# Kernel optimization log

Hardware: AMD Instinct MI355X
Metric: run time of the kernel (lower is better)

The kernel has to match this reference:

```python
import jax, jax.numpy as jnp
import numpy as np
from jax import lax

NPG = 61      # nodes (electrodes) per graph, hard-coded by 61*hidden reshape
B = 128       # graphs per batch
L = 160       # raw signal length -> final conv length 1
NF = 64       # num_features
HC = 128      # hidden_channels
NCLS = 4


def setup_inputs() -> dict:
    key = jax.random.key(0)
    ks = jax.random.split(key, 16)
    N = B * NPG
    # fully-connected (no self-loops) edges within each graph -> 3660 edges/graph
    a = np.repeat(np.arange(NPG), NPG)
    b = np.tile(np.arange(NPG), NPG)
    m = a != b
    sl, dl = a[m], b[m]
    off = (np.arange(B) * NPG)[:, None]
    edge_index = np.stack([(sl[None] + off).ravel(), (dl[None] + off).ravel()]).astype(np.int64)
    batch = np.repeat(np.arange(B), NPG).astype(np.int64)

    def rn(k, shape, fan_in):
        return jax.random.normal(k, shape, jnp.float32) / np.sqrt(fan_in).astype(np.float32)

    return dict(
        x=jax.random.normal(ks[0], (N, L), jnp.float32),
        edge_index=jnp.asarray(edge_index),
        batch=jnp.asarray(batch),
        edge_features=jax.random.normal(ks[1], (edge_index.shape[1], 3), jnp.float32),
        conv_w0=rn(ks[2], (NF, 1, 7), 7.0), conv_b0=jnp.zeros((NF,), jnp.float32),
        conv_w1=rn(ks[3], (NF, NF, 5), NF * 5.0), conv_b1=jnp.zeros((NF,), jnp.float32),
        conv_w2=rn(ks[4], (NF, NF, 3), NF * 3.0), conv_b2=jnp.zeros((NF,), jnp.float32),
        bn1_g=jnp.ones((NF,), jnp.float32), bn1_b=jnp.zeros((NF,), jnp.float32),
        g_w0=rn(ks[5], (NF, HC), float(NF)), g_b0=jnp.zeros((HC,), jnp.float32),
        g_w1=rn(ks[6], (HC, HC), float(HC)), g_b1=jnp.zeros((HC,), jnp.float32),
        g_w2=rn(ks[7], (HC, HC), float(HC)), g_b2=jnp.zeros((HC,), jnp.float32),
        bn2_g=jnp.ones((HC,), jnp.float32), bn2_b=jnp.zeros((HC,), jnp.float32),
        lin_w0=rn(ks[8], (NPG * HC, HC), float(NPG * HC)), lin_b0=jnp.zeros((HC,), jnp.float32),
        lin_w1=rn(ks[9], (HC, HC), float(HC)), lin_b1=jnp.zeros((HC,), jnp.float32),
        lin_w2=rn(ks[10], (HC, NCLS), float(HC)), lin_b2=jnp.zeros((NCLS,), jnp.float32),
        edge_w=rn(ks[11], (3, 1), 3.0), edge_b=jnp.zeros((1,), jnp.float32),
    )


def _conv1d(x, w, b, pad):
    # x: [N, Cin, L], w: [Cout, Cin, K]
    y = lax.conv_general_dilated(x, w, (1,), [(pad, pad)], dimension_numbers=('NCH', 'OIH', 'NCH'))
    return y + b[None, :, None]


def _maxpool7(x):
    n = x.shape[-1] // 7
    return x[..., : n * 7].reshape(x.shape[0], x.shape[1], n, 7).max(-1)


def _bn(x, g, b):
    # BatchNorm1d in training mode: biased batch statistics
    m = x.mean(0)
    v = x.var(0)
    return (x - m) * lax.rsqrt(v + 1e-5) * g + b


def _forward(x, edge_features, conv_w0, conv_b0, conv_w1, conv_b1, conv_w2, conv_b2,
             bn1_g, bn1_b, g_w0, g_b0, g_w1, g_b1, g_w2, g_b2, bn2_g, bn2_b,
             lin_w0, lin_b0, lin_w1, lin_b1, lin_w2, lin_b2, edge_w, edge_b,
             edge_index, batch):
    N = x.shape[0]
    nb = N // NPG  # == batch.max()+1 for contiguous graph layout
    # tanh-gated edge weights
    ew = jnp.tanh(edge_features @ edge_w + edge_b)            # [E, 1]
    # Conv1d feature extractor: [N,1,160] -> [N,NF,1]
    h = x[:, None, :]
    h = _maxpool7(jax.nn.relu(_conv1d(h, conv_w0, conv_b0, 0)))   # [N,NF,22]
    h = jax.nn.relu(_conv1d(h, conv_w1, conv_b1, 2))               # [N,NF,22]
    h = _maxpool7(h)                                               # [N,NF,3]
    h = _conv1d(h, conv_w2, conv_b2, 0)[:, :, 0]                   # [N,NF]
    h = _bn(h, bn1_g, bn1_b)
    # Edge-weighted GCN hops (MyzConv): lin -> gather src -> scale -> scatter-add dst
    src, dst = edge_index[0], edge_index[1]
    for w, bs, act in ((g_w0, g_b0, True), (g_w1, g_b1, True), (g_w2, g_b2, False)):
        hw = h @ w + bs                                            # [N,HC]
        msg = ew * hw[src]                                         # [E,HC]
        h = jax.ops.segment_sum(msg, dst, num_segments=N)
        if act:
            h = jax.nn.relu(h)
    h = _bn(h, bn2_g, bn2_b)
    # MLP classifier over concatenated node features per graph
    h = h.reshape(nb, NPG * HC)
    h = jax.nn.relu(h @ lin_w0 + lin_b0)
    h = jax.nn.relu(h @ lin_w1 + lin_b1)
    h = h @ lin_w2 + lin_b2
    return jax.nn.log_softmax(h, -1), ew.reshape(nb, -1).T


def reference(x, edge_index, batch, edge_features, conv_w0, conv_b0, conv_w1, conv_b1,
              conv_w2, conv_b2, bn1_g, bn1_b, g_w0, g_b0, g_w1, g_b1, g_w2, g_b2,
              bn2_g, bn2_b, lin_w0, lin_b0, lin_w1, lin_b1, lin_w2, lin_b2, edge_w, edge_b):
    return _forward(x, edge_features, conv_w0, conv_b0, conv_w1, conv_b1, conv_w2, conv_b2,
                    bn1_g, bn1_b, g_w0, g_b0, g_w1, g_b1, g_w2, g_b2, bn2_g, bn2_b,
                    lin_w0, lin_b0, lin_w1, lin_b1, lin_w2, lin_b2, edge_w, edge_b,
                    edge_index, batch)
```

## Files before the change

### kernel.cpp

```cpp
#include <hip/hip_runtime.h>
#include <math.h>

#define NPGN 61
#define NGRAPH 128
#define NNODES (NPGN*NGRAPH)
#define EPG 3660

typedef float float4v __attribute__((ext_vector_type(4)));
typedef short bf16x8 __attribute__((ext_vector_type(8)));
typedef unsigned short u16;

__device__ __forceinline__ u16 f2bf(float v){
  union { float f; unsigned u; } x; x.f = v;
  unsigned r = (x.u + 0x7FFFu + ((x.u >> 16) & 1u)) >> 16;
  return (u16)r;
}
__device__ __forceinline__ float bf2f(unsigned u){
  union { unsigned u; float f; } x; x.u = u << 16;
  return x.f;
}

__global__ __launch_bounds__(256) void k_prep(const float* __restrict__ w0,
    const float* __restrict__ w1, const float* __restrict__ w2,
    const float* __restrict__ gw0, const float* __restrict__ gw1, const float* __restrict__ gw2,
    const float* __restrict__ lw0,
    float* __restrict__ w0t, u16* __restrict__ w1b, u16* __restrict__ w2b,
    u16* __restrict__ gwt0, u16* __restrict__ gwt1, u16* __restrict__ gwt2,
    u16* __restrict__ lw0t){
  __shared__ __align__(16) u16 tile[32*132];
  int b = blockIdx.x, tid = threadIdx.x;
  if (b < 290){
    int idx = b*256 + tid;
    if (idx < 20480){
      int f = idx / 320, r = idx - f*320;
      int kk = r >> 6, c = r & 63;
      w1b[idx] = f2bf(w1[f*320 + c*5 + kk]);
    } else if (idx < 32768){
      int j = idx - 20480; w2b[j] = f2bf(w2[j]);
    } else if (idx < 40960){
      int j = idx - 32768; int jj = j >> 6, k = j & 63; gwt0[j] = f2bf(gw0[k*128 + jj]);
    } else if (idx < 57344){
      int j = idx - 40960; int jj = j >> 7, k = j & 127; gwt1[j] = f2bf(gw1[k*128 + jj]);
    } else if (idx < 73728){
      int j = idx - 57344; int jj = j >> 7, k = j & 127; gwt2[j] = f2bf(gw2[k*128 + jj]);
    } else if (idx < 74176){
      int j = idx - 73728; int k = j >> 6, f = j & 63; w0t[j] = w0[f*7 + k];
    }
  } else {
    int bb = b - 290;
    int i = bb >> 2, oq = bb & 3;
    for (int idx = tid; idx < 4096; idx += 256){
      int k = idx >> 5, ol = idx & 31;
      tile[ol*132 + k] = f2bf(lw0[((size_t)i*128 + k)*128 + oq*32 + ol]);
    }
    __syncthreads();
    unsigned* dst = (unsigned*)lw0t;
    for (int idx = tid; idx < 2048; idx += 256){
      int ol = idx >> 6, kw = idx & 63;
      unsigned v = (unsigned)tile[ol*132 + 2*kw] | ((unsigned)tile[ol*132 + 2*kw + 1] << 16);
      dst[((size_t)i*128 + oq*32 + ol)*64 + kw] = v;
    }
  }
}

#define A0T_STR 72
#define C1_STR 24
#define NB 4
__global__ __launch_bounds__(256) void k_conv(const float* __restrict__ x,
    const float* __restrict__ w0t, const float* __restrict__ b0,
    const u16* __restrict__ w1b, const float* __restrict__ b1,
    const u16* __restrict__ w2b, const float* __restrict__ b2,
    float* __restrict__ h0, float* __restrict__ stat1p){
  int w = threadIdx.x >> 6, lane = threadIdx.x & 63;
  int tid = threadIdx.x;
  int q = lane >> 4, r16 = lane & 15;
  __shared__ __align__(16) float xs[NB][160];
  __shared__ __align__(16) u16 a0t[NB][36*A0T_STR];
  __shared__ __align__(16) u16 c1s[NB][64*C1_STR];
  __shared__ __align__(16) u16 a1k[NB][208];

  {
    const float* xb = x + (size_t)blockIdx.x*NB*160;
    float* xsf = &xs[0][0];
    #pragma unroll
    for (int idx = tid; idx < NB*160; idx += 256) xsf[idx] = xb[idx];
  }

  bf16x8 wf1[10], wf2[6];
  #pragma unroll
  for (int ks = 0; ks < 10; ks++)
    wf1[ks] = *(const bf16x8*)(w1b + (16*w + r16)*320 + ks*32 + q*8);
  #pragma unroll
  for (int ks = 0; ks < 6; ks++)
    wf2[ks] = *(const bf16x8*)(w2b + (16*w + r16)*192 + ks*32 + q*8);
  float4 b1v = *(const float4*)(b1 + 16*w + 4*q);
  float4 b2v = *(const float4*)(b2 + 16*w + 4*q);

  float w0r[7];
  #pragma unroll
  for (int k = 0; k < 7; k++) w0r[k] = w0t[k*64 + lane];
  float b0f = b0[lane];

  #pragma unroll
  for (int i2 = 0; i2 < 6; i2++){
    int rp = (i2 < 2) ? i2 : 22 + i2;
    a0t[w][rp*A0T_STR + lane] = 0;
  }
  __syncthreads();

  for (int j = w; j < 44; j += 4){
    int n = j / 11, qp = j - n*11;
    const float* xsp = &xs[n][0];
    float win[20];
// ... 20 lines not shown
  __syncthreads();

  #pragma unroll 1
  for (int n = 0; n < NB; n++){
    float4v acc0 = {0.f,0.f,0.f,0.f}, acc1 = {0.f,0.f,0.f,0.f};
    #pragma unroll
    for (int ks = 0; ks < 10; ks++){
      int kk = ks >> 1;
      int cbase = (ks & 1)*32 + q*8;
      bf16x8 bv0 = *(const bf16x8*)(&a0t[n][(r16 + kk)*A0T_STR + cbase]);
      bf16x8 bv1 = *(const bf16x8*)(&a0t[n][(r16 + 16 + kk)*A0T_STR + cbase]);
      acc0 = __builtin_amdgcn_mfma_f32_16x16x32_bf16(wf1[ks], bv0, acc0, 0, 0, 0);
      acc1 = __builtin_amdgcn_mfma_f32_16x16x32_bf16(wf1[ks], bv1, acc1, 0, 0, 0);
    }
    #pragma unroll
    for (int reg = 0; reg < 4; reg++){
      int m = 16*w + q*4 + reg;
      float bv_ = ((const float*)&b1v)[reg];
      c1s[n][m*C1_STR + r16] = f2bf(fmaxf(acc0[reg] + bv_, 0.f));
      if (r16 <= 4)
        c1s[n][m*C1_STR + 16 + r16] = f2bf(fmaxf(acc1[reg] + bv_, 0.f));
    }
  }
  __syncthreads();

  {
    const u16* c1 = &c1s[w][0];
    bf16x8 f0 = *(const bf16x8*)(c1 + lane*C1_STR);
    bf16x8 f1 = *(const bf16x8*)(c1 + lane*C1_STR + 8);
    bf16x8 f2 = *(const bf16x8*)(c1 + lane*C1_STR + 16);
    float v[24];
    #pragma unroll
    for (int j = 0; j < 8; j++){
      v[j]    = bf2f((u16)f0[j]);
      v[8+j]  = bf2f((u16)f1[j]);
      v[16+j] = bf2f((u16)f2[j]);
    }
    #pragma unroll
    for (int t = 0; t < 3; t++){
      float m = v[t*7];
      #pragma unroll
      for (int r = 1; r < 7; r++) m = fmaxf(m, v[t*7+r]);
      a1k[w][lane*3 + t] = f2bf(m);
    }
  }
  __syncthreads();

  float4v sacc = {0.f,0.f,0.f,0.f}, qacc = {0.f,0.f,0.f,0.f};
  #pragma unroll 1
  for (int n = 0; n < NB; n++){
    float4v acc2 = {0.f,0.f,0.f,0.f};
    #pragma unroll
    for (int ks = 0; ks < 6; ks++){
      bf16x8 bs = *(const bf16x8*)(&a1k[n][ks*32 + q*8]);
      acc2 = __builtin_amdgcn_mfma_f32_16x16x32_bf16(wf2[ks], bs, acc2, 0, 0, 0);
    }
    if (r16 == 0){
      int nn = blockIdx.x*NB + n;
      #pragma unroll
      for (int reg = 0; reg < 4; reg++){
        int f = 16*w + 4*q + reg;
        float v = acc2[reg] + ((const float*)&b2v)[reg];
        h0[(size_t)nn*64 + f] = v;
        sacc[reg] += v;
        qacc[reg] += v*v;
      }
    }
  }

  if (r16 == 0){
    int bkt = blockIdx.x & 31;
    #pragma unroll
    for (int reg = 0; reg < 4; reg++){
      int f = 16*w + 4*q + reg;
      atomicAdd(&stat1p[bkt*128 + f], sacc[reg]);
      atomicAdd(&stat1p[bkt*128 + 64 + f], qacc[reg]);
    }
  }
}

#define EW_STR 72
#define HS_STR 136
#define HWT_STR 72
__global__ __launch_bounds__(512) void k_gnn(const float* __restrict__ h0,
    const float* __restrict__ stat1p,
    const float* __restrict__ bn1g, const float* __restrict__ bn1b,
    const u16* __restrict__ gwt0, const float* __restrict__ gb0,
    const u16* __restrict__ gwt1, const float* __restrict__ gb1,
    const u16* __restrict__ gwt2, const float* __restrict__ gb2,
    const float* __restrict__ ef, const float* __restrict__ eww,
    const float* __restrict__ ewb, float* __restrict__ out2,
    u16* __restrict__ hB, float* __restrict__ stat2p){
  int g = blockIdx.x, tid = threadIdx.x;
  int w = tid >> 6, lane = tid & 63, q = lane >> 4, r16 = lane & 15;
  int dt = w & 3, jh = w >> 2;
  __shared__ u16 hs[64*HS_STR];
  __shared__ u16 hwT[128*HWT_STR];
  __shared__ u16 ewl[64*EW_STR];
  __shared__ float bsc[64], bsh[64];
  __shared__ float st2[256];

  bf16x8 af0[2], af1[4], af2[4];
  #pragma unroll
  for (int ks = 0; ks < 2; ks++)
    af0[ks] = *(const bf16x8*)(gwt0 + (16*w + r16)*64 + ks*32 + q*8);
  #pragma unroll
  for (int ks = 0; ks < 4; ks++)
    af1[ks] = *(const bf16x8*)(gwt1 + (16*w + r16)*128 + ks*32 + q*8);
  #pragma unroll
  for (int ks = 0; ks < 4; ks++)
    af2[ks] = *(const bf16x8*)(gwt2 + (16*w + r16)*128 + ks*32 + q*8);
  float4 b40 = *(const float4*)(gb0 + 16*w + 4*q);
  float4 b41 = *(const float4*)(gb1 + 16*w + 4*q);
  float4 b42 = *(const float4*)(gb2 + 16*w + 4*q);

  if (tid < 64){
    float s = 0.f, s2 = 0.f;
    #pragma unroll
    for (int r = 0; r < 32; r++){
      s  += stat1p[r*128 + tid];
      s2 += stat1p[r*128 + 64 + tid];
    }
    float m = s*(1.f/NNODES), v = s2*(1.f/NNODES) - m*m;
    float sc = rsqrtf(v + 1e-5f)*bn1g[tid];
    bsc[tid] = sc; bsh[tid] = bn1b[tid] - m*sc;
  }
  if (tid < 256) st2[tid] = 0.f;
  {
    unsigned* td = (unsigned*)ewl;
    for (int idx = tid; idx < 64*EW_STR/2; idx += 512) td[idx] = 0;
  }
  {
    unsigned* hsd = (unsigned*)hs;
    for (int idx = tid; idx < 3*(HS_STR/2); idx += 512){
      int rr = 61 + idx/(HS_STR/2), cc = idx%(HS_STR/2);
      hsd[rr*(HS_STR/2) + cc] = 0;
    }
  }
  __syncthreads();

  {
    float v0 = eww[0], v1 = eww[1], v2 = eww[2], bb = ewb[0];
    const float* efg = ef + (size_t)g*EPG*3;
    for (int idx = tid; idx < EPG; idx += 512){
      const float* p = efg + idx*3;
      float v = tanhf(p[0]*v0 + p[1]*v1 + p[2]*v2 + bb);
      int s = idx/60, r = idx - s*60;
      int d = r + (r >= s ? 1 : 0);
      ewl[d*EW_STR + s] = f2bf(v);
      out2[(size_t)idx*128 + g] = v;
    }
  }
  {
    unsigned* hsd = (unsigned*)hs;
    for (int idx = tid; idx < 61*32; idx += 512){
      int i = idx >> 5, kw = idx & 31;
      float2 hv = *(const float2*)(h0 + ((size_t)g*61 + i)*64 + kw*2);
      int k0 = kw*2;
      float a = hv.x*bsc[k0] + bsh[k0];
      float b = hv.y*bsc[k0+1] + bsh[k0+1];
      hsd[i*(HS_STR/2) + kw] = (unsigned)f2bf(a) | ((unsigned)f2bf(b) << 16);
    }
  }
  __syncthreads();
  bf16x8 ewf[2];
  #pragma unroll
  for (int ks = 0; ks < 2; ks++)
    ewf[ks] = *(const bf16x8*)(ewl + (16*dt + r16)*EW_STR + ks*32 + q*8);

  #pragma unroll
  for (int nt = 0; nt < 4; nt++){
    float4v acc = {b40.x, b40.y, b40.z, b40.w};
    #pragma unroll
    for (int ks = 0; ks < 2; ks++){
      bf16x8 bv = *(const bf16x8*)(hs + (nt*16 + r16)*HS_STR + ks*32 + q*8);
      acc = __builtin_amdgcn_mfma_f32_16x16x32_bf16(af0[ks], bv, acc, 0, 0, 0);
    }
    #pragma unroll
    for (int r = 0; r < 4; r++)
      hwT[(16*w + 4*q + r)*HWT_STR + nt*16 + r16] = f2bf(acc[r]);
  }
  __syncthreads();
  #pragma unroll
  for (int nt = 0; nt < 4; nt++){
    int j = (jh*4 + nt)*16;
    float4v acc = {0.f,0.f,0.f,0.f};
    #pragma unroll
    for (int ks = 0; ks < 2; ks++){
      bf16x8 bv = *(const bf16x8*)(hwT + (j + r16)*HWT_STR + ks*32 + q*8);
      acc = __builtin_amdgcn_mfma_f32_16x16x32_bf16(ewf[ks], bv, acc, 0, 0, 0);
    }
    #pragma unroll
    for (int r = 0; r < 4; r++){
      int d = 16*dt + 4*q + r;
      hs[d*HS_STR + j + r16] = f2bf(fmaxf(acc[r], 0.f));
    }
  }
  __syncthreads();

  #pragma unroll
  for (int nt = 0; nt < 4; nt++){
    float4v acc = {b41.x, b41.y, b41.z, b41.w};
    #pragma unroll
    for (int ks = 0; ks < 4; ks++){
      bf16x8 bv = *(const bf16x8*)(hs + (nt*16 + r16)*HS_STR + ks*32 + q*8);
      acc = __builtin_amdgcn_mfma_f32_16x16x32_bf16(af1[ks], bv, acc, 0, 0, 0);
    }
    #pragma unroll
    for (int r = 0; r < 4; r++)
      hwT[(16*w + 4*q + r)*HWT_STR + nt*16 + r16] = f2bf(acc[r]);
  }
  __syncthreads();
  #pragma unroll
  for (int nt = 0; nt < 4; nt++){
    int j = (jh*4 + nt)*16;
    float4v acc = {0.f,0.f,0.f,0.f};
    #pragma unroll
    for (int ks = 0; ks < 2; ks++){
      bf16x8 bv = *(const bf16x8*)(hwT + (j + r16)*HWT_STR + ks*32 + q*8);
      acc = __builtin_amdgcn_mfma_f32_16x16x32_bf16(ewf[ks], bv, acc, 0, 0, 0);
    }
    #pragma unroll
    for (int r = 0; r < 4; r++){
      int d = 16*dt + 4*q + r;
      hs[d*HS_STR + j + r16] = f2bf(fmaxf(acc[r], 0.f));
    }
  }
  __syncthreads();

  #pragma unroll
  for (int nt = 0; nt < 4; nt++){
    float4v acc = {b42.x, b42.y, b42.z, b42.w};
    #pragma unroll
    for (int ks = 0; ks < 4; ks++){
      bf16x8 bv = *(const bf16x8*)(hs + (nt*16 + r16)*HS_STR + ks*32 + q*8);
      acc = __builtin_amdgcn_mfma_f32_16x16x32_bf16(af2[ks], bv, acc, 0, 0, 0);
    }
    #pragma unroll
    for (int r = 0; r < 4; r++)
      hwT[(16*w + 4*q + r)*HWT_STR + nt*16 + r16] = f2bf(acc[r]);
  }
  __syncthreads();
  #pragma unroll
  for (int nt = 0; nt < 4; nt++){
    int j = (jh*4 + nt)*16;
    float4v acc = {0.f,0.f,0.f,0.f};
    #pragma unroll
    for (int ks = 0; ks < 2; ks++){
      bf16x8 bv = *(const bf16x8*)(hwT + (j + r16)*HWT_STR + ks*32 + q*8);
      acc = __builtin_amdgcn_mfma_f32_16x16x32_bf16(ewf[ks], bv, acc, 0, 0, 0);
    }
    float cs = 0.f, cq = 0.f;
    #pragma unroll
    for (int r = 0; r < 4; r++){
      int d = 16*dt + 4*q + r;
      if (d < 61){
        float v = acc[r];
        hB[((size_t)g*61 + d)*128 + j + r16] = f2bf(v);
        cs += v; cq += v*v;
      }
    }
    int col = j + r16;
    atomicAdd(&st2[col], cs);
    atomicAdd(&st2[128 + col], cq);
  }
  __syncthreads();
  if (tid < 256) stat2p[(size_t)tid*128 + g] = st2[tid];
}

#define AS_STR 136
__global__ __launch_bounds__(256) void k_mlp0(const u16* __restrict__ hB,
    const float* __restrict__ stat2p,
    const float* __restrict__ bn2g, const float* __restrict__ bn2b,
    const u16* __restrict__ lw0t, float* __restrict__ y0pre){
  int bi = blockIdx.x; int i = bi >> 2, sub = bi & 3;
  int oh = sub & 1, gh = sub >> 1;
  int tid = threadIdx.x, w = tid >> 6, lane = tid & 63, q = lane >> 4, r16 = lane & 15;
  __shared__ u16 As[64*AS_STR];
  __shared__ float sc2[128], sh2[128];
  if (tid < 128){
    float4v sa = {0,0,0,0}, sb = {0,0,0,0};
    #pragma unroll
    for (int r = 0; r < 32; r++){
      sa += *(const float4v*)(stat2p + (size_t)tid*128 + r*4);
      sb += *(const float4v*)(stat2p + (size_t)(128 + tid)*128 + r*4);
    }
    float s = sa[0]+sa[1]+sa[2]+sa[3], s2 = sb[0]+sb[1]+sb[2]+sb[3];
    float m = s*(1.f/NNODES), v = s2*(1.f/NNODES) - m*m;
    float sc = rsqrtf(v + 1e-5f)*bn2g[tid];
    sc2[tid] = sc; sh2[tid] = bn2b[tid] - m*sc;
  }
  __syncthreads();
  {
    const unsigned* hbd = (const unsigned*)hB;
    unsigned* asd = (unsigned*)As;
    for (int idx = tid; idx < 4096; idx += 256){
      int gg = gh*64 + (idx >> 6), kw = idx & 63;
      unsigned pv = hbd[((size_t)gg*61 + i)*64 + kw];
      int k0 = kw*2;
      float a = bf2f(pv & 0xffffu)*sc2[k0] + sh2[k0];
      float b = bf2f(pv >> 16)*sc2[k0+1] + sh2[k0+1];
      asd[(idx >> 6)*(AS_STR/2) + kw] = (unsigned)f2bf(a) | ((unsigned)f2bf(b) << 16);
    }
  }
  __syncthreads();
  const u16* wbase = lw0t + ((size_t)i*128 + oh*64)*128;
  bf16x8 af[4];
  #pragma unroll
  for (int ks = 0; ks < 4; ks++)
    af[ks] = *(const bf16x8*)(As + (16*w + r16)*AS_STR + ks*32 + q*8);
  #pragma unroll
  for (int nt = 0; nt < 4; nt++){
    float4v acc = {0.f,0.f,0.f,0.f};
    #pragma unroll
    for (int ks = 0; ks < 4; ks++){
      bf16x8 bv = *(const bf16x8*)(wbase + (size_t)(nt*16 + r16)*128 + ks*32 + q*8);
      acc = __builtin_amdgcn_mfma_f32_16x16x32_bf16(af[ks], bv, acc, 0, 0, 0);
    }
    #pragma unroll
    for (int r = 0; r < 4; r++){
      int g = gh*64 + 16*w + 4*q + r;
      atomicAdd(&y0pre[(size_t)g*128 + oh*64 + nt*16 + r16], acc[r]);
    }
  }
}

__global__ __launch_bounds__(128) void k_mlp1(const float* __restrict__ y0pre,
    const float* __restrict__ lb0, const float* __restrict__ W1,
    const float* __restrict__ lb1, const float* __restrict__ W2,
    const float* __restrict__ lb2, float* __restrict__ out){
  int g = blockIdx.x, o = threadIdx.x;
  __shared__ float y0[128], y1[128], red[128];
  y0[o] = fmaxf(y0pre[(size_t)g*128 + o] + lb0[o], 0.f);
  __syncthreads();
  float a = lb1[o];
  #pragma unroll 8
  for (int k = 0; k < 128; k++) a += y0[k]*W1[k*128 + o];
  y1[o] = fmaxf(a, 0.f);
  __syncthreads();
  int c = o & 3, kb = o >> 2;
  float a2 = 0.f;
  #pragma unroll
  for (int j = 0; j < 4; j++){
    int k = kb + 32*j;
    a2 += y1[k]*W2[k*4 + c];
  }
  red[o] = a2;
  __syncthreads();
  #pragma unroll
  for (int off = 64; off >= 4; off >>= 1){
    if (o < off) red[o] += red[o + off];
    __syncthreads();
  }
  if (o == 0){
    float v0 = red[0]+lb2[0], v1 = red[1]+lb2[1], v2 = red[2]+lb2[2], v3 = red[3]+lb2[3];
    float m = fmaxf(fmaxf(v0,v1), fmaxf(v2,v3));
    float lse = m + logf(expf(v0-m)+expf(v1-m)+expf(v2-m)+expf(v3-m));
    out[g*4+0]=v0-lse; out[g*4+1]=v1-lse; out[g*4+2]=v2-lse; out[g*4+3]=v3-lse;
  }
}

extern "C" void kernel_launch(void* const* d_in, const int* in_sizes, int n_in,
                              void* d_out, int out_size, void* d_ws, size_t ws_size,
                              hipStream_t stream){
  const float* x    = (const float*)d_in[0];
  const float* ef   = (const float*)d_in[3];
  const float* cw0  = (const float*)d_in[4];
  const float* cb0  = (const float*)d_in[5];
  const float* cw1  = (const float*)d_in[6];
  const float* cb1  = (const float*)d_in[7];
  const float* cw2  = (const float*)d_in[8];
  const float* cb2  = (const float*)d_in[9];
  const float* bn1g = (const float*)d_in[10];
  const float* bn1b = (const float*)d_in[11];
  const float* gw0  = (const float*)d_in[12];
  const float* gb0  = (const float*)d_in[13];
  const float* gw1  = (const float*)d_in[14];
  const float* gb1  = (const float*)d_in[15];
  const float* gw2  = (const float*)d_in[16];
  const float* gb2  = (const float*)d_in[17];
  const float* bn2g = (const float*)d_in[18];
  const float* bn2b = (const float*)d_in[19];
  const float* lw0  = (const float*)d_in[20];
  const float* lb0  = (const float*)d_in[21];
  const float* lw1  = (const float*)d_in[22];
  const float* lb1  = (const float*)d_in[23];
  const float* lw2  = (const float*)d_in[24];
  const float* lb2  = (const float*)d_in[25];
  const float* eww  = (const float*)d_in[26];
  const float* ewb  = (const float*)d_in[27];
  float* out = (float*)d_out;

  float* ws   = (float*)d_ws;
  float* w1s  = ws;
  float* w2s  = w1s + 10240;
  float* w0t  = w2s + 6144;
  float* gws0 = w0t + 448;
  float* gws1 = gws0 + 4096;
  float* gws2 = gws1 + 8192;
  float* h0   = gws2 + 8192;
  float* hBs  = h0 + 499712;
  float* lw0s = hBs + 499712;
  float* accs = lw0s + 499712;

  u16* w1b    = (u16*)w1s;
  u16* w2b    = (u16*)w2s;
  u16* gwt0   = (u16*)gws0;
  u16* gwt1   = (u16*)gws1;
  u16* gwt2   = (u16*)gws2;
  u16* hB     = (u16*)hBs;
  u16* lw0t   = (u16*)lw0s;
  float* stat1p = accs;
  float* y0pre  = accs + 4096;
  float* stat2p = accs + 20480;

  hipMemsetAsync(accs, 0, 20480*sizeof(float), stream);
  k_prep <<<534, 256, 0, stream>>>(cw0, cw1, cw2, gw0, gw1, gw2, lw0,
                                   w0t, w1b, w2b, gwt0, gwt1, gwt2, lw0t);
  k_conv <<<NNODES/NB, 256, 0, stream>>>(x, w0t, cb0, w1b, cb1, w2b, cb2, h0, stat1p);
  k_gnn  <<<NGRAPH, 512, 0, stream>>>(h0, stat1p, bn1g, bn1b,
                                      gwt0, gb0, gwt1, gb1, gwt2, gb2,
                                      ef, eww, ewb, out + 512, hB, stat2p);
  k_mlp0 <<<NPGN*4, 256, 0, stream>>>(hB, stat2p, bn2g, bn2b, lw0t, y0pre);
  k_mlp1 <<<NGRAPH, 128, 0, stream>>>(y0pre, lb0, lw1, lb1, lw2, lb2, out);
}
```

Measured before the change: 199.1 us.

## Fuse GNN and MLP stages into one cooperative kernel with grid syncs

The separate GNN, first-MLP and second-MLP kernels are merged into a single cooperative kernel with 244 blocks, separated by grid-wide barriers. The accumulator memset moves into extra blocks of the prep kernel. The aim is to remove launch gaps and the memset launch. The costs are grid-sync latency, idle blocks during the GNN and final phases, and larger shared-memory use per block from the union of all stages, which may limit co-residency.

```diff
diff --git a/kernel.cpp b/kernel.cpp
--- a/kernel.cpp
+++ b/kernel.cpp
@@ -1,5 +1,8 @@
 #include <hip/hip_runtime.h>
+#include <hip/hip_cooperative_groups.h>
 #include <math.h>
+
+namespace cg = cooperative_groups;
 
 #define NPGN 61
 #define NGRAPH 128
@@ -26,9 +29,14 @@
     const float* __restrict__ lw0,
     float* __restrict__ w0t, u16* __restrict__ w1b, u16* __restrict__ w2b,
     u16* __restrict__ gwt0, u16* __restrict__ gwt1, u16* __restrict__ gwt2,
-    u16* __restrict__ lw0t){
+    u16* __restrict__ lw0t, float* __restrict__ accs){
   __shared__ __align__(16) u16 tile[32*132];
   int b = blockIdx.x, tid = threadIdx.x;
+  if (b >= 534){
+    int idx = (b - 534)*256 + tid;
+    if (idx < 20480) accs[idx] = 0.f;
+    return;
+  }
   if (b < 290){
     int idx = b*256 + tid;
     if (idx < 20480){
@@ -215,281 +223,295 @@
 #define EW_STR 72
 #define HS_STR 136
 #define HWT_STR 72
-__global__ __launch_bounds__(512) void k_gnn(const float* __restrict__ h0,
+#define AS_STR 136
+__global__ __launch_bounds__(512) void k_tail(const float* __restrict__ h0,
     const float* __restrict__ stat1p,
     const float* __restrict__ bn1g, const float* __restrict__ bn1b,
     const u16* __restrict__ gwt0, const float* __restrict__ gb0,
     const u16* __restrict__ gwt1, const float* __restrict__ gb1,
     const u16* __restrict__ gwt2, const float* __restrict__ gb2,
     const float* __restrict__ ef, const float* __restrict__ eww,
-    const float* __restrict__ ewb, float* __restrict__ out2,
-    u16* __restrict__ hB, float* __restrict__ stat2p){
-  int g = blockIdx.x, tid = threadIdx.x;
+    const float* __restrict__ ewb, u16* __restrict__ hB,
+    float* __restrict__ stat2p,
+    const float* __restrict__ bn2g, const float* __restrict__ bn2b,
+    const u16* __restrict__ lw0t, float* __restrict__ y0pre,
+    const float* __restrict__ lb0, const float* __restrict__ W1,
+    const float* __restrict__ lb1, const float* __restrict__ W2,
+    const float* __restrict__ lb2, float* __restrict__ out){
+  int tid = threadIdx.x;
   int w = tid >> 6, lane = tid & 63, q = lane >> 4, r16 = lane & 15;
-  int dt = w & 3, jh = w >> 2;
   __shared__ u16 hs[64*HS_STR];
   __shared__ u16 hwT[128*HWT_STR];
   __shared__ u16 ewl[64*EW_STR];
   __shared__ float bsc[64], bsh[64];
   __shared__ float st2[256];
-
-  bf16x8 af0[2], af1[4], af2[4];
-  #pragma unroll
-  for (int ks = 0; ks < 2; ks++)
-    af0[ks] = *(const bf16x8*)(gwt0 + (16*w + r16)*64 + ks*32 + q*8);
-  #pragma unroll
-  for (int ks = 0; ks < 4; ks++)
-    af1[ks] = *(const bf16x8*)(gwt1 + (16*w + r16)*128 + ks*32 + q*8);
-  #pragma unroll
-  for (int ks = 0; ks < 4; ks++)
-    af2[ks] = *(const bf16x8*)(gwt2 + (16*w + r16)*128 + ks*32 + q*8);
-  float4 b40 = *(const float4*)(gb0 + 16*w + 4*q);
-  float4 b41 = *(const float4*)(gb1 + 16*w + 4*q);
-  float4 b42 = *(const float4*)(gb2 + 16*w + 4*q);
-
-  if (tid < 64){
-    float s = 0.f, s2 = 0.f;
-    #pragma unroll
-    for (int r = 0; r < 32; r++){
-      s  += stat1p[r*128 + tid];
-      s2 += stat1p[r*128 + 64 + tid];
-    }
-    float m = s*(1.f/NNODES), v = s2*(1.f/NNODES) - m*m;
-    float sc = rsqrtf(v + 1e-5f)*bn1g[tid];
-    bsc[tid] = sc; bsh[tid] = bn1b[tid] - m*sc;
-  }
-  if (tid < 256) st2[tid] = 0.f;
-  {
-    unsigned* td = (unsigned*)ewl;
-    for (int idx = tid; idx < 64*EW_STR/2; idx += 512) td[idx] = 0;
-  }
-  {
-    unsigned* hsd = (unsigned*)hs;
-    for (int idx = tid; idx < 3*(HS_STR/2); idx += 512){
-      int rr = 61 + idx/(HS_STR/2), cc = idx%(HS_STR/2);
-      hsd[rr*(HS_STR/2) + cc] = 0;
-    }
-  }
-  __syncthreads();
-
-  {
-    float v0 = eww[0], v1 = eww[1], v2 = eww[2], bb = ewb[0];
-    const float* efg = ef + (size_t)g*EPG*3;
-    for (int idx = tid; idx < EPG; idx += 512){
-      const float* p = efg + idx*3;
-      float v = tanhf(p[0]*v0 + p[1]*v1 + p[2]*v2 + bb);
-      int s = idx/60, r = idx - s*60;
-      int d = r + (r >= s ? 1 : 0);
-      ewl[d*EW_STR + s] = f2bf(v);
-      out2[(size_t)idx*128 + g] = v;
-    }
-  }
-  {
-    unsigned* hsd = (unsigned*)hs;
-    for (int idx = tid; idx < 61*32; idx += 512){
-      int i = idx >> 5, kw = idx & 31;
-      float2 hv = *(const float2*)(h0 + ((size_t)g*61 + i)*64 + kw*2);
-      int k0 = kw*2;
-      float a = hv.x*bsc[k0] + bsh[k0];
-      float b = hv.y*bsc[k0+1] + bsh[k0+1];
-      hsd[i*(HS_STR/2) + kw] = (unsigned)f2bf(a) | ((unsigned)f2bf(b) << 16);
-    }
-  }
-  __syncthreads();
-  bf16x8 ewf[2];
-  #pragma unroll
-  for (int ks = 0; ks < 2; ks++)
-    ewf[ks] = *(const bf16x8*)(ewl + (16*dt + r16)*EW_STR + ks*32 + q*8);
-
-  #pragma unroll
-  for (int nt = 0; nt < 4; nt++){
-    float4v acc = {b40.x, b40.y, b40.z, b40.w};
-    #pragma unroll
-    for (int ks = 0; ks < 2; ks++){
-      bf16x8 bv = *(const bf16x8*)(hs + (nt*16 + r16)*HS_STR + ks*32 + q*8);
-      acc = __builtin_amdgcn_mfma_f32_16x16x32_bf16(af0[ks], bv, acc, 0, 0, 0);
-    }
-    #pragma unroll
-    for (int r = 0; r < 4; r++)
-      hwT[(16*w + 4*q + r)*HWT_STR + nt*16 + r16] = f2bf(acc[r]);
-  }
-  __syncthreads();
-  #pragma unroll
-  for (int nt = 0; nt < 4; nt++){
-    int j = (jh*4 + nt)*16;
-    float4v acc = {0.f,0.f,0.f,0.f};
-    #pragma unroll
-    for (int ks = 0; ks < 2; ks++){
-      bf16x8 bv = *(const bf16x8*)(hwT + (j + r16)*HWT_STR + ks*32 + q*8);
-      acc = __builtin_amdgcn_mfma_f32_16x16x32_bf16(ewf[ks], bv, acc, 0, 0, 0);
-    }
-    #pragma unroll
-    for (int r = 0; r < 4; r++){
-      int d = 16*dt + 4*q + r;
-      hs[d*HS_STR + j + r16] = f2bf(fmaxf(acc[r], 0.f));
-    }
-  }
-  __syncthreads();
-
-  #pragma unroll
-  for (int nt = 0; nt < 4; nt++){
-    float4v acc = {b41.x, b41.y, b41.z, b41.w};
-    #pragma unroll
-    for (int ks = 0; ks < 4; ks++){
-      bf16x8 bv = *(const bf16x8*)(hs + (nt*16 + r16)*HS_STR + ks*32 + q*8);
-      acc = __builtin_amdgcn_mfma_f32_16x16x32_bf16(af1[ks], bv, acc, 0, 0, 0);
-    }
-    #pragma unroll
-    for (int r = 0; r < 4; r++)
-      hwT[(16*w + 4*q + r)*HWT_STR + nt*16 + r16] = f2bf(acc[r]);
-  }
-  __syncthreads();
-  #pragma unroll
-  for (int nt = 0; nt < 4; nt++){
-    int j = (jh*4 + nt)*16;
-    float4v acc = {0.f,0.f,0.f,0.f};
-    #pragma unroll
-    for (int ks = 0; ks < 2; ks++){
-      bf16x8 bv = *(const bf16x8*)(hwT + (j + r16)*HWT_STR + ks*32 + q*8);
-      acc = __builtin_amdgcn_mfma_f32_16x16x32_bf16(ewf[ks], bv, acc, 0, 0, 0);
-    }
-    #pragma unroll
-    for (int r = 0; r < 4; r++){
-      int d = 16*dt + 4*q + r;
-      hs[d*HS_STR + j + r16] = f2bf(fmaxf(acc[r], 0.f));
-    }
-  }
-  __syncthreads();
-
-  #pragma unroll
-  for (int nt = 0; nt < 4; nt++){
-    float4v acc = {b42.x, b42.y, b42.z, b42.w};
-    #pragma unroll
-    for (int ks = 0; ks < 4; ks++){
-      bf16x8 bv = *(const bf16x8*)(hs + (nt*16 + r16)*HS_STR + ks*32 + q*8);
-      acc = __builtin_amdgcn_mfma_f32_16x16x32_bf16(af2[ks], bv, acc, 0, 0, 0);
-    }
-    #pragma unroll
-    for (int r = 0; r < 4; r++)
-      hwT[(16*w + 4*q + r)*HWT_STR + nt*16 + r16] = f2bf(acc[r]);
-  }
-  __syncthreads();
-  #pragma unroll
-  for (int nt = 0; nt < 4; nt++){
-    int j = (jh*4 + nt)*16;
-    float4v acc = {0.f,0.f,0.f,0.f};
-    #pragma unroll
-    for (int ks = 0; ks < 2; ks++){
-      bf16x8 bv = *(const bf16x8*)(hwT + (j + r16)*HWT_STR + ks*32 + q*8);
-      acc = __builtin_amdgcn_mfma_f32_16x16x32_bf16(ewf[ks], bv, acc, 0, 0, 0);
-    }
-    float cs = 0.f, cq = 0.f;
-    #pragma unroll
-    for (int r = 0; r < 4; r++){
-      int d = 16*dt + 4*q + r;
-      if (d < 61){
-        float v = acc[r];
-        hB[((size_t)g*61 + d)*128 + j + r16] = f2bf(v);
-        cs += v; cq += v*v;
-      }
-    }
-    int col = j + r16;
-    atomicAdd(&st2[col], cs);
-    atomicAdd(&st2[128 + col], cq);
-  }
-  __syncthreads();
-  if (tid < 256) stat2p[(size_t)tid*128 + g] = st2[tid];
-}
-
-#define AS_STR 136
-__global__ __launch_bounds__(256) void k_mlp0(const u16* __restrict__ hB,
-    const float* __restrict__ stat2p,
-    const float* __restrict__ bn2g, const float* __restrict__ bn2b,
-    const u16* __restrict__ lw0t, float* __restrict__ y0pre){
-  int bi = blockIdx.x; int i = bi >> 2, sub = bi & 3;
-  int oh = sub & 1, gh = sub >> 1;
-  int tid = threadIdx.x, w = tid >> 6, lane = tid & 63, q = lane >> 4, r16 = lane & 15;
   __shared__ u16 As[64*AS_STR];
   __shared__ float sc2[128], sh2[128];
-  if (tid < 128){
-    float4v sa = {0,0,0,0}, sb = {0,0,0,0};
-    #pragma unroll
-    for (int r = 0; r < 32; r++){
-      sa += *(const float4v*)(stat2p + (size_t)tid*128 + r*4);
-      sb += *(const float4v*)(stat2p + (size_t)(128 + tid)*128 + r*4);
-    }
-    float s = sa[0]+sa[1]+sa[2]+sa[3], s2 = sb[0]+sb[1]+sb[2]+sb[3];
-    float m = s*(1.f/NNODES), v = s2*(1.f/NNODES) - m*m;
-    float sc = rsqrtf(v + 1e-5f)*bn2g[tid];
-    sc2[tid] = sc; sh2[tid] = bn2b[tid] - m*sc;
-  }
-  __syncthreads();
+  __shared__ float y0[128], y1[128], red[128];
+  float* out2 = out + 512;
+
+  if (blockIdx.x < NGRAPH){
+    int g = blockIdx.x;
+    int dt = w & 3, jh = w >> 2;
+
+    bf16x8 af0[2], af1[4], af2[4];
+    #pragma unroll
+    for (int ks = 0; ks < 2; ks++)
+      af0[ks] = *(const bf16x8*)(gwt0 + (16*w + r16)*64 + ks*32 + q*8);
+    #pragma unroll
+    for (int ks = 0; ks < 4; ks++)
+      af1[ks] = *(const bf16x8*)(gwt1 + (16*w + r16)*128 + ks*32 + q*8);
+    #pragma unroll
+    for (int ks = 0; ks < 4; ks++)
+      af2[ks] = *(const bf16x8*)(gwt2 + (16*w + r16)*128 + ks*32 + q*8);
+    float4 b40 = *(const float4*)(gb0 + 16*w + 4*q);
+    float4 b41 = *(const float4*)(gb1 + 16*w + 4*q);
+    float4 b42 = *(const float4*)(gb2 + 16*w + 4*q);
+
+    if (tid < 64){
+      float s = 0.f, s2 = 0.f;
+      #pragma unroll
+      for (int r = 0; r < 32; r++){
+        s  += stat1p[r*128 + tid];
+        s2 += stat1p[r*128 + 64 + tid];
+      }
+      float m = s*(1.f/NNODES), v = s2*(1.f/NNODES) - m*m;
+      float sc = rsqrtf(v + 1e-5f)*bn1g[tid];
+      bsc[tid] = sc; bsh[tid] = bn1b[tid] - m*sc;
+    }
+    if (tid < 256) st2[tid] = 0.f;
+    {
+      unsigned* td = (unsigned*)ewl;
+      for (int idx = tid; idx < 64*EW_STR/2; idx += 512) td[idx] = 0;
+    }
+    {
+      unsigned* hsd = (unsigned*)hs;
+      for (int idx = tid; idx < 3*(HS_STR/2); idx += 512){
+        int rr = 61 + idx/(HS_STR/2), cc = idx%(HS_STR/2);
+        hsd[rr*(HS_STR/2) + cc] = 0;
+      }
+    }
+    __syncthreads();
+
+    {
+      float v0 = eww[0], v1 = eww[1], v2 = eww[2], bb = ewb[0];
+      const float* efg = ef + (size_t)g*EPG*3;
+      for (int idx = tid; idx < EPG; idx += 512){
+        const float* p = efg + idx*3;
+        float v = tanhf(p[0]*v0 + p[1]*v1 + p[2]*v2 + bb);
+        int s = idx/60, r = idx - s*60;
+        int d = r + (r >= s ? 1 : 0);
+        ewl[d*EW_STR + s] = f2bf(v);
+        out2[(size_t)idx*128 + g] = v;
+      }
+    }
+    {
+      unsigned* hsd = (unsigned*)hs;
+      for (int idx = tid; idx < 61*32; idx += 512){
+        int i = idx >> 5, kw = idx & 31;
+        float2 hv = *(const float2*)(h0 + ((size_t)g*61 + i)*64 + kw*2);
+        int k0 = kw*2;
+        float a = hv.x*bsc[k0] + bsh[k0];
+        float b = hv.y*bsc[k0+1] + bsh[k0+1];
+        hsd[i*(HS_STR/2) + kw] = (unsigned)f2bf(a) | ((unsigned)f2bf(b) << 16);
+      }
+    }
+    __syncthreads();
+    bf16x8 ewf[2];
+    #pragma unroll
+    for (int ks = 0; ks < 2; ks++)
+      ewf[ks] = *(const bf16x8*)(ewl + (16*dt + r16)*EW_STR + ks*32 + q*8);
+
+    #pragma unroll
+    for (int nt = 0; nt < 4; nt++){
+      float4v acc = {b40.x, b40.y, b40.z, b40.w};
+      #pragma unroll
+      for (int ks = 0; ks < 2; ks++){
+        bf16x8 bv = *(const bf16x8*)(hs + (nt*16 + r16)*HS_STR + ks*32 + q*8);
+        acc = __builtin_amdgcn_mfma_f32_16x16x32_bf16(af0[ks], bv, acc, 0, 0, 0);
+      }
+      #pragma unroll
+      for (int r = 0; r < 4; r++)
+        hwT[(16*w + 4*q + r)*HWT_STR + nt*16 + r16] = f2bf(acc[r]);
+    }
+    __syncthreads();
+    #pragma unroll
+    for (int nt = 0; nt < 4; nt++){
+      int j = (jh*4 + nt)*16;
+      float4v acc = {0.f,0.f,0.f,0.f};
+      #pragma unroll
+      for (int ks = 0; ks < 2; ks++){
+        bf16x8 bv = *(const bf16x8*)(hwT + (j + r16)*HWT_STR + ks*32 + q*8);
+        acc = __builtin_amdgcn_mfma_f32_16x16x32_bf16(ewf[ks], bv, acc, 0, 0, 0);
+      }
+      #pragma unroll
+      for (int r = 0; r < 4; r++){
+        int d = 16*dt + 4*q + r;
+        hs[d*HS_STR + j + r16] = f2bf(fmaxf(acc[r], 0.f));
+      }
+    }
+    __syncthreads();
+
+    #pragma unroll
+    for (int nt = 0; nt < 4; nt++){
+      float4v acc = {b41.x, b41.y, b41.z, b41.w};
+      #pragma unroll
+      for (int ks = 0; ks < 4; ks++){
+        bf16x8 bv = *(const bf16x8*)(hs + (nt*16 + r16)*HS_STR + ks*32 + q*8);
+        acc = __builtin_amdgcn_mfma_f32_16x16x32_bf16(af1[ks], bv, acc, 0, 0, 0);
+      }
+      #pragma unroll
+      for (int r = 0; r < 4; r++)
+        hwT[(16*w + 4*q + r)*HWT_STR + nt*16 + r16] = f2bf(acc[r]);
+    }
+    __syncthreads();
+    #pragma unroll
+    for (int nt = 0; nt < 4; nt++){
+      int j = (jh*4 + nt)*16;
+      float4v acc = {0.f,0.f,0.f,0.f};
+      #pragma unroll
+      for (int ks = 0; ks < 2; ks++){
+        bf16x8 bv = *(const bf16x8*)(hwT + (j + r16)*HWT_STR + ks*32 + q*8);
+        acc = __builtin_amdgcn_mfma_f32_16x16x32_bf16(ewf[ks], bv, acc, 0, 0, 0);
+      }
+      #pragma unroll
+      for (int r = 0; r < 4; r++){
+        int d = 16*dt + 4*q + r;
+        hs[d*HS_STR + j + r16] = f2bf(fmaxf(acc[r], 0.f));
+      }
+    }
+    __syncthreads();
+
+    #pragma unroll
+    for (int nt = 0; nt < 4; nt++){
+      float4v acc = {b42.x, b42.y, b42.z, b42.w};
+      #pragma unroll
+      for (int ks = 0; ks < 4; ks++){
+        bf16x8 bv = *(const bf16x8*)(hs + (nt*16 + r16)*HS_STR + ks*32 + q*8);
+        acc = __builtin_amdgcn_mfma_f32_16x16x32_bf16(af2[ks], bv, acc, 0, 0, 0);
+      }
+      #pragma unroll
+      for (int r = 0; r < 4; r++)
+        hwT[(16*w + 4*q + r)*HWT_STR + nt*16 + r16] = f2bf(acc[r]);
+    }
+    __syncthreads();
+    #pragma unroll
+    for (int nt = 0; nt < 4; nt++){
+      int j = (jh*4 + nt)*16;
+      float4v acc = {0.f,0.f,0.f,0.f};
+      #pragma unroll
+      for (int ks = 0; ks < 2; ks++){
+        bf16x8 bv = *(const bf16x8*)(hwT + (j + r16)*HWT_STR + ks*32 + q*8);
+        acc = __builtin_amdgcn_mfma_f32_16x16x32_bf16(ewf[ks], bv, acc, 0, 0, 0);
+      }
+      float cs = 0.f, cq = 0.f;
+      #pragma unroll
+      for (int r = 0; r < 4; r++){
+        int d = 16*dt + 4*q + r;
+        if (d < 61){
+          float v = acc[r];
+          hB[((size_t)g*61 + d)*128 + j + r16] = f2bf(v);
+          cs += v; cq += v*v;
+        }
+      }
+      int col = j + r16;
+      atomicAdd(&st2[col], cs);
+      atomicAdd(&st2[128 + col], cq);
+    }
+    __syncthreads();
+    if (tid < 256) stat2p[(size_t)tid*128 + g] = st2[tid];
+  }
+
+  cg::this_grid().sync();
+
   {
-    const unsigned* hbd = (const unsigned*)hB;
-    unsigned* asd = (unsigned*)As;
-    for (int idx = tid; idx < 4096; idx += 256){
-      int gg = gh*64 + (idx >> 6), kw = idx & 63;
-      unsigned pv = hbd[((size_t)gg*61 + i)*64 + kw];
-      int k0 = kw*2;
-      float a = bf2f(pv & 0xffffu)*sc2[k0] + sh2[k0];
-      float b = bf2f(pv >> 16)*sc2[k0+1] + sh2[k0+1];
-      asd[(idx >> 6)*(AS_STR/2) + kw] = (unsigned)f2bf(a) | ((unsigned)f2bf(b) << 16);
-    }
-  }
-  __syncthreads();
-  const u16* wbase = lw0t + ((size_t)i*128 + oh*64)*128;
-  bf16x8 af[4];
-  #pragma unroll
-  for (int ks = 0; ks < 4; ks++)
-    af[ks] = *(const bf16x8*)(As + (16*w + r16)*AS_STR + ks*32 + q*8);
-  #pragma unroll
-  for (int nt = 0; nt < 4; nt++){
-    float4v acc = {0.f,0.f,0.f,0.f};
-    #pragma unroll
-    for (int ks = 0; ks < 4; ks++){
-      bf16x8 bv = *(const bf16x8*)(wbase + (size_t)(nt*16 + r16)*128 + ks*32 + q*8);
-      acc = __builtin_amdgcn_mfma_f32_16x16x32_bf16(af[ks], bv, acc, 0, 0, 0);
-    }
-    #pragma unroll
-    for (int r = 0; r < 4; r++){
-      int g = gh*64 + 16*w + 4*q + r;
-      atomicAdd(&y0pre[(size_t)g*128 + oh*64 + nt*16 + r16], acc[r]);
-    }
-  }
-}
-
-__global__ __launch_bounds__(128) void k_mlp1(const float* __restrict__ y0pre,
-    const float* __restrict__ lb0, const float* __restrict__ W1,
-    const float* __restrict__ lb1, const float* __restrict__ W2,
-    const float* __restrict__ lb2, float* __restrict__ out){
-  int g = blockIdx.x, o = threadIdx.x;
-  __shared__ float y0[128], y1[128], red[128];
-  y0[o] = fmaxf(y0pre[(size_t)g*128 + o] + lb0[o], 0.f);
-  __syncthreads();
-  float a = lb1[o];
-  #pragma unroll 8
-  for (int k = 0; k < 128; k++) a += y0[k]*W1[k*128 + o];
-  y1[o] = fmaxf(a, 0.f);
-  __syncthreads();
-  int c = o & 3, kb = o >> 2;
-  float a2 = 0.f;
-  #pragma unroll
-  for (int j = 0; j < 4; j++){
-    int k = kb + 32*j;
-    a2 += y1[k]*W2[k*4 + c];
-  }
-  red[o] = a2;
-  __syncthreads();
-  #pragma unroll
-  for (int off = 64; off >= 4; off >>= 1){
-    if (o < off) red[o] += red[o + off];
-    __syncthreads();
-  }
-  if (o == 0){
-    float v0 = red[0]+lb2[0], v1 = red[1]+lb2[1], v2 = red[2]+lb2[2], v3 = red[3]+lb2[3];
-    float m = fmaxf(fmaxf(v0,v1), fmaxf(v2,v3));
-    float lse = m + logf(expf(v0-m)+expf(v1-m)+expf(v2-m)+expf(v3-m));
-    out[g*4+0]=v0-lse; out[g*4+1]=v1-lse; out[g*4+2]=v2-lse; out[g*4+3]=v3-lse;
+    int nh = w >> 2, w4 = w & 3;
+    if (tid < 128){
+      float4v sa = {0,0,0,0}, sb = {0,0,0,0};
+      #pragma unroll
+      for (int r = 0; r < 32; r++){
+        sa += *(const float4v*)(stat2p + (size_t)tid*128 + r*4);
+        sb += *(const float4v*)(stat2p + (size_t)(128 + tid)*128 + r*4);
+      }
+      float s = sa[0]+sa[1]+sa[2]+sa[3], s2 = sb[0]+sb[1]+sb[2]+sb[3];
+      float m = s*(1.f/NNODES), v = s2*(1.f/NNODES) - m*m;
+      float sc = rsqrtf(v + 1e-5f)*bn2g[tid];
+      sc2[tid] = sc; sh2[tid] = bn2b[tid] - m*sc;
+    }
+    int vb = blockIdx.x;
+    int i = vb >> 2, sub = vb & 3;
+    int oh = sub & 1, gh = sub >> 1;
+    __syncthreads();
+    {
+      const unsigned* hbd = (const unsigned*)hB;
+      unsigned* asd = (unsigned*)As;
+      for (int idx = tid; idx < 4096; idx += 512){
+        int gg = gh*64 + (idx >> 6), kw = idx & 63;
+        unsigned pv = hbd[((size_t)gg*61 + i)*64 + kw];
+        int k0 = kw*2;
+        float a = bf2f(pv & 0xffffu)*sc2[k0] + sh2[k0];
+        float b = bf2f(pv >> 16)*sc2[k0+1] + sh2[k0+1];
+        asd[(idx >> 6)*(AS_STR/2) + kw] = (unsigned)f2bf(a) | ((unsigned)f2bf(b) << 16);
+      }
+    }
+    __syncthreads();
+    const u16* wbase = lw0t + ((size_t)i*128 + oh*64)*128;
+    bf16x8 af[4];
+    #pragma unroll
+    for (int ks = 0; ks < 4; ks++)
+      af[ks] = *(const bf16x8*)(As + (16*w4 + r16)*AS_STR + ks*32 + q*8);
+    #pragma unroll
+    for (int t = 0; t < 2; t++){
+      int nt = nh*2 + t;
+      float4v acc = {0.f,0.f,0.f,0.f};
+      #pragma unroll
+      for (int ks = 0; ks < 4; ks++){
+        bf16x8 bv = *(const bf16x8*)(wbase + (size_t)(nt*16 + r16)*128 + ks*32 + q*8);
+        acc = __builtin_amdgcn_mfma_f32_16x16x32_bf16(af[ks], bv, acc, 0, 0, 0);
+      }
+      #pragma unroll
+      for (int r = 0; r < 4; r++){
+        int g = gh*64 + 16*w4 + 4*q + r;
+        atomicAdd(&y0pre[(size_t)g*128 + oh*64 + nt*16 + r16], acc[r]);
+      }
+    }
+  }
+
+  cg::this_grid().sync();
+
+  if (blockIdx.x < NGRAPH){
+    int g = blockIdx.x, o = tid;
+    if (o < 128) y0[o] = fmaxf(y0pre[(size_t)g*128 + o] + lb0[o], 0.f);
+    __syncthreads();
+    if (o < 128){
+      float a = lb1[o];
+      #pragma unroll 8
+      for (int k = 0; k < 128; k++) a += y0[k]*W1[k*128 + o];
+      y1[o] = fmaxf(a, 0.f);
+    }
+    __syncthreads();
+    if (o < 128){
+      int c = o & 3, kb = o >> 2;
+      float a2 = 0.f;
+      #pragma unroll
+      for (int j = 0; j < 4; j++){
+        int k = kb + 32*j;
+        a2 += y1[k]*W2[k*4 + c];
+      }
+      red[o] = a2;
+    }
+    __syncthreads();
+    #pragma unroll
+    for (int off = 64; off >= 4; off >>= 1){
+      if (o < off) red[o] += red[o + off];
+      __syncthreads();
+    }
+    if (o == 0){
+      float v0 = red[0]+lb2[0], v1 = red[1]+lb2[1], v2 = red[2]+lb2[2], v3 = red[3]+lb2[3];
+      float m = fmaxf(fmaxf(v0,v1), fmaxf(v2,v3));
+      float lse = m + logf(expf(v0-m)+expf(v1-m)+expf(v2-m)+expf(v3-m));
+      out[g*4+0]=v0-lse; out[g*4+1]=v1-lse; out[g*4+2]=v2-lse; out[g*4+3]=v3-lse;
+    }
   }
 }
 
@@ -547,13 +569,18 @@
   float* y0pre  = accs + 4096;
   float* stat2p = accs + 20480;
 
-  hipMemsetAsync(accs, 0, 20480*sizeof(float), stream);
-  k_prep <<<534, 256, 0, stream>>>(cw0, cw1, cw2, gw0, gw1, gw2, lw0,
-                                   w0t, w1b, w2b, gwt0, gwt1, gwt2, lw0t);
+  k_prep <<<614, 256, 0, stream>>>(cw0, cw1, cw2, gw0, gw1, gw2, lw0,
+                                   w0t, w1b, w2b, gwt0, gwt1, gwt2, lw0t, accs);
   k_conv <<<NNODES/NB, 256, 0, stream>>>(x, w0t, cb0, w1b, cb1, w2b, cb2, h0, stat1p);
-  k_gnn  <<<NGRAPH, 512, 0, stream>>>(h0, stat1p, bn1g, bn1b,
-                                      gwt0, gb0, gwt1, gb1, gwt2, gb2,
-                                      ef, eww, ewb, out + 512, hB, stat2p);
-  k_mlp0 <<<NPGN*4, 256, 0, stream>>>(hB, stat2p, bn2g, bn2b, lw0t, y0pre);
-  k_mlp1 <<<NGRAPH, 128, 0, stream>>>(y0pre, lb0, lw1, lb1, lw2, lb2, out);
+
+  void* args[] = {
+    (void*)&h0, (void*)&stat1p, (void*)&bn1g, (void*)&bn1b,
+    (void*)&gwt0, (void*)&gb0, (void*)&gwt1, (void*)&gb1,
+    (void*)&gwt2, (void*)&gb2, (void*)&ef, (void*)&eww, (void*)&ewb,
+    (void*)&hB, (void*)&stat2p, (void*)&bn2g, (void*)&bn2b,
+    (void*)&lw0t, (void*)&y0pre, (void*)&lb0, (void*)&lw1,
+    (void*)&lb1, (void*)&lw2, (void*)&lb2, (void*)&out
+  };
+  hipLaunchCooperativeKernel((void*)k_tail, dim3(NPGN*4), dim3(512),
+                             args, 0, stream);
 }
```

Measured after the change: 292.1 us. 46.7% more time.

## Fuse MLP kernels with last-block completion counter and fold memset into prep

Applied to the files above, without the earlier changes.

Replaces the hipMemsetAsync with extra zeroing blocks in k_prep, and merges k_mlp0 and k_mlp1 into one kernel. Each block now processes four node indices and accumulates in registers, which cuts the number of y0pre atomics by four. The last block to finish, found through an atomic counter, runs the small classifier MLP for all graphs. This removes two launches and the memset, but the 64-block grid lowers parallelism in the first layer, and the tail MLP now runs serially in a single block.

```diff
diff --git a/kernel.cpp b/kernel.cpp
--- a/kernel.cpp
+++ b/kernel.cpp
@@ -26,9 +26,14 @@
     const float* __restrict__ lw0,
     float* __restrict__ w0t, u16* __restrict__ w1b, u16* __restrict__ w2b,
     u16* __restrict__ gwt0, u16* __restrict__ gwt1, u16* __restrict__ gwt2,
-    u16* __restrict__ lw0t){
+    u16* __restrict__ lw0t, float* __restrict__ accs){
   __shared__ __align__(16) u16 tile[32*132];
   int b = blockIdx.x, tid = threadIdx.x;
+  if (b >= 534){
+    int idx = (b - 534)*256 + tid;
+    if (idx < 20736) accs[idx] = 0.f;
+    return;
+  }
   if (b < 290){
     int idx = b*256 + tid;
     if (idx < 20480){
@@ -402,15 +407,22 @@
 }
 
 #define AS_STR 136
-__global__ __launch_bounds__(256) void k_mlp0(const u16* __restrict__ hB,
+__global__ __launch_bounds__(256) void k_mlp01(const u16* __restrict__ hB,
     const float* __restrict__ stat2p,
     const float* __restrict__ bn2g, const float* __restrict__ bn2b,
-    const u16* __restrict__ lw0t, float* __restrict__ y0pre){
-  int bi = blockIdx.x; int i = bi >> 2, sub = bi & 3;
+    const u16* __restrict__ lw0t, float* __restrict__ y0pre,
+    unsigned* __restrict__ cnt,
+    const float* __restrict__ lb0, const float* __restrict__ W1,
+    const float* __restrict__ lb1, const float* __restrict__ W2,
+    const float* __restrict__ lb2, float* __restrict__ out){
+  int bi = blockIdx.x; int ig = bi >> 2, sub = bi & 3;
   int oh = sub & 1, gh = sub >> 1;
   int tid = threadIdx.x, w = tid >> 6, lane = tid & 63, q = lane >> 4, r16 = lane & 15;
   __shared__ u16 As[64*AS_STR];
   __shared__ float sc2[128], sh2[128];
+  __shared__ float y0[2][128], y1[2][128], red[2][128];
+  __shared__ unsigned sflag;
+
   if (tid < 128){
     float4v sa = {0,0,0,0}, sb = {0,0,0,0};
     #pragma unroll
@@ -423,73 +435,92 @@
     float sc = rsqrtf(v + 1e-5f)*bn2g[tid];
     sc2[tid] = sc; sh2[tid] = bn2b[tid] - m*sc;
   }
-  __syncthreads();
-  {
-    const unsigned* hbd = (const unsigned*)hB;
-    unsigned* asd = (unsigned*)As;
-    for (int idx = tid; idx < 4096; idx += 256){
-      int gg = gh*64 + (idx >> 6), kw = idx & 63;
-      unsigned pv = hbd[((size_t)gg*61 + i)*64 + kw];
-      int k0 = kw*2;
-      float a = bf2f(pv & 0xffffu)*sc2[k0] + sh2[k0];
-      float b = bf2f(pv >> 16)*sc2[k0+1] + sh2[k0+1];
-      asd[(idx >> 6)*(AS_STR/2) + kw] = (unsigned)f2bf(a) | ((unsigned)f2bf(b) << 16);
-    }
-  }
-  __syncthreads();
-  const u16* wbase = lw0t + ((size_t)i*128 + oh*64)*128;
-  bf16x8 af[4];
-  #pragma unroll
-  for (int ks = 0; ks < 4; ks++)
-    af[ks] = *(const bf16x8*)(As + (16*w + r16)*AS_STR + ks*32 + q*8);
-  #pragma unroll
-  for (int nt = 0; nt < 4; nt++){
-    float4v acc = {0.f,0.f,0.f,0.f};
-    #pragma unroll
-    for (int ks = 0; ks < 4; ks++){
-      bf16x8 bv = *(const bf16x8*)(wbase + (size_t)(nt*16 + r16)*128 + ks*32 + q*8);
-      acc = __builtin_amdgcn_mfma_f32_16x16x32_bf16(af[ks], bv, acc, 0, 0, 0);
-    }
+
+  float4v acc[4];
+  #pragma unroll
+  for (int nt = 0; nt < 4; nt++) acc[nt] = (float4v){0.f,0.f,0.f,0.f};
+
+  #pragma unroll 1
+  for (int t = 0; t < 4; t++){
+    int i = ig*4 + t;
+    __syncthreads();
+    if (i < 61){
+      const unsigned* hbd = (const unsigned*)hB;
+      unsigned* asd = (unsigned*)As;
+      for (int idx = tid; idx < 4096; idx += 256){
+        int gg = gh*64 + (idx >> 6), kw = idx & 63;
+        unsigned pv = hbd[((size_t)gg*61 + i)*64 + kw];
+        int k0 = kw*2;
+        float a = bf2f(pv & 0xffffu)*sc2[k0] + sh2[k0];
+        float b = bf2f(pv >> 16)*sc2[k0+1] + sh2[k0+1];
+        asd[(idx >> 6)*(AS_STR/2) + kw] = (unsigned)f2bf(a) | ((unsigned)f2bf(b) << 16);
+      }
+    }
+    __syncthreads();
+    if (i < 61){
+      const u16* wbase = lw0t + ((size_t)i*128 + oh*64)*128;
+      bf16x8 af[4];
+      #pragma unroll
+      for (int ks = 0; ks < 4; ks++)
+        af[ks] = *(const bf16x8*)(As + (16*w + r16)*AS_STR + ks*32 + q*8);
+      #pragma unroll
+      for (int nt = 0; nt < 4; nt++){
+        #pragma unroll
+        for (int ks = 0; ks < 4; ks++){
+          bf16x8 bv = *(const bf16x8*)(wbase + (size_t)(nt*16 + r16)*128 + ks*32 + q*8);
+          acc[nt] = __builtin_amdgcn_mfma_f32_16x16x32_bf16(af[ks], bv, acc[nt], 0, 0, 0);
+        }
+      }
+    }
+  }
+
+  #pragma unroll
+  for (int nt = 0; nt < 4; nt++){
     #pragma unroll
     for (int r = 0; r < 4; r++){
       int g = gh*64 + 16*w + 4*q + r;
-      atomicAdd(&y0pre[(size_t)g*128 + oh*64 + nt*16 + r16], acc[r]);
-    }
-  }
-}
-
-__global__ __launch_bounds__(128) void k_mlp1(const float* __restrict__ y0pre,
-    const float* __restrict__ lb0, const float* __restrict__ W1,
-    const float* __restrict__ lb1, const float* __restrict__ W2,
-    const float* __restrict__ lb2, float* __restrict__ out){
-  int g = blockIdx.x, o = threadIdx.x;
-  __shared__ float y0[128], y1[128], red[128];
-  y0[o] = fmaxf(y0pre[(size_t)g*128 + o] + lb0[o], 0.f);
-  __syncthreads();
-  float a = lb1[o];
-  #pragma unroll 8
-  for (int k = 0; k < 128; k++) a += y0[k]*W1[k*128 + o];
-  y1[o] = fmaxf(a, 0.f);
-  __syncthreads();
-  int c = o & 3, kb = o >> 2;
-  float a2 = 0.f;
-  #pragma unroll
-  for (int j = 0; j < 4; j++){
-    int k = kb + 32*j;
-    a2 += y1[k]*W2[k*4 + c];
-  }
-  red[o] = a2;
-  __syncthreads();
-  #pragma unroll
-  for (int off = 64; off >= 4; off >>= 1){
-    if (o < off) red[o] += red[o + off];
-    __syncthreads();
-  }
-  if (o == 0){
-    float v0 = red[0]+lb2[0], v1 = red[1]+lb2[1], v2 = red[2]+lb2[2], v3 = red[3]+lb2[3];
-    float m = fmaxf(fmaxf(v0,v1), fmaxf(v2,v3));
-    float lse = m + logf(expf(v0-m)+expf(v1-m)+expf(v2-m)+expf(v3-m));
-    out[g*4+0]=v0-lse; out[g*4+1]=v1-lse; out[g*4+2]=v2-lse; out[g*4+3]=v3-lse;
+      atomicAdd(&y0pre[(size_t)g*128 + oh*64 + nt*16 + r16], acc[nt][r]);
+    }
+  }
+
+  __threadfence();
+  __syncthreads();
+  if (tid == 0) sflag = atomicAdd(cnt, 1u);
+  __syncthreads();
+  if (sflag != 63u) return;
+
+  int sg = tid >> 7, o = tid & 127;
+  for (int g = sg; g < NGRAPH; g += 2){
+    float yv = atomicAdd(&y0pre[(size_t)g*128 + o], 0.f);
+    y0[sg][o] = fmaxf(yv + lb0[o], 0.f);
+    __syncthreads();
+    float a = lb1[o];
+    #pragma unroll 8
+    for (int k = 0; k < 128; k++) a += y0[sg][k]*W1[k*128 + o];
+    y1[sg][o] = fmaxf(a, 0.f);
+    __syncthreads();
+    int c = o & 3, kb = o >> 2;
+    float a2 = 0.f;
+    #pragma unroll
+    for (int j = 0; j < 4; j++){
+      int k = kb + 32*j;
+      a2 += y1[sg][k]*W2[k*4 + c];
+    }
+    red[sg][o] = a2;
+    __syncthreads();
+    #pragma unroll
+    for (int off = 64; off >= 4; off >>= 1){
+      if (o < off) red[sg][o] += red[sg][o + off];
+      __syncthreads();
+    }
+    if (o == 0){
+      float v0 = red[sg][0]+lb2[0], v1 = red[sg][1]+lb2[1];
+      float v2 = red[sg][2]+lb2[2], v3 = red[sg][3]+lb2[3];
+      float m = fmaxf(fmaxf(v0,v1), fmaxf(v2,v3));
+      float lse = m + logf(expf(v0-m)+expf(v1-m)+expf(v2-m)+expf(v3-m));
+      out[g*4+0]=v0-lse; out[g*4+1]=v1-lse; out[g*4+2]=v2-lse; out[g*4+3]=v3-lse;
+    }
+    __syncthreads();
   }
 }
 
@@ -545,15 +576,15 @@
   u16* lw0t   = (u16*)lw0s;
   float* stat1p = accs;
   float* y0pre  = accs + 4096;
-  float* stat2p = accs + 20480;
-
-  hipMemsetAsync(accs, 0, 20480*sizeof(float), stream);
-  k_prep <<<534, 256, 0, stream>>>(cw0, cw1, cw2, gw0, gw1, gw2, lw0,
-                                   w0t, w1b, w2b, gwt0, gwt1, gwt2, lw0t);
+  unsigned* cnt = (unsigned*)(accs + 20480);
+  float* stat2p = accs + 20736;
+
+  k_prep <<<615, 256, 0, stream>>>(cw0, cw1, cw2, gw0, gw1, gw2, lw0,
+                                   w0t, w1b, w2b, gwt0, gwt1, gwt2, lw0t, accs);
   k_conv <<<NNODES/NB, 256, 0, stream>>>(x, w0t, cb0, w1b, cb1, w2b, cb2, h0, stat1p);
   k_gnn  <<<NGRAPH, 512, 0, stream>>>(h0, stat1p, bn1g, bn1b,
                                       gwt0, gb0, gwt1, gb1, gwt2, gb2,
                                       ef, eww, ewb, out + 512, hB, stat2p);
-  k_mlp0 <<<NPGN*4, 256, 0, stream>>>(hB, stat2p, bn2g, bn2b, lw0t, y0pre);
-  k_mlp1 <<<NGRAPH, 128, 0, stream>>>(y0pre, lb0, lw1, lb1, lw2, lb2, out);
-}
+  k_mlp01<<<64, 256, 0, stream>>>(hB, stat2p, bn2g, bn2b, lw0t, y0pre, cnt,
+                                  lb0, lw1, lb1, lw2, lb2, out);
+}
```

Result: slower. 412.6 us (+107.2%).
